# Kernel tuning notes

Measured on AMD Instinct MI355X. Metric: run time of the kernel, lower is better.

Reference implementation:

```python
import jax, jax.numpy as jnp
import numpy as np
from jax import lax

D_MODEL = 512
D_STATE = 64
D_CONV = 4
EXPAND = 2
HEADDIM = 64
D_INNER = EXPAND * D_MODEL          # 1024
NHEADS = D_INNER // HEADDIM         # 16
CONV_DIM = D_INNER + 2 * D_STATE    # 1152 (x, B, C go through depthwise conv)
D_PROJ = 2 * D_INNER + 2 * D_STATE + NHEADS  # 2192
EPS = 1e-5


def silu(x):
    return x * jax.nn.sigmoid(x)


def layernorm(x, w, b):
    mu = jnp.mean(x, axis=-1, keepdims=True)
    var = jnp.mean((x - mu) ** 2, axis=-1, keepdims=True)
    return (x - mu) * lax.rsqrt(var + EPS) * w + b


def mamba2(x, in_w, conv_w, conv_b, dt_bias, A_log, D_h, mnorm_w, out_w):
    """Faithful Mamba2 forward (sequential selective-scan form of SSD).
    x: [B, L, D_MODEL]"""
    Bsz, L, _ = x.shape
    zxbcdt = x @ in_w  # [B, L, D_PROJ]
    z = zxbcdt[..., :D_INNER]
    xBC = zxbcdt[..., D_INNER:D_INNER + CONV_DIM]
    dt = zxbcdt[..., -NHEADS:]

    # causal depthwise conv1d over sequence, then SiLU
    xBC_pad = jnp.pad(xBC, ((0, 0), (D_CONV - 1, 0), (0, 0)))
    xBC = lax.conv_general_dilated(
        xBC_pad, conv_w, window_strides=(1,), padding='VALID',
        dimension_numbers=('NWC', 'WIO', 'NWC'), feature_group_count=CONV_DIM)
    xBC = silu(xBC + conv_b)

    xh = xBC[..., :D_INNER].reshape(Bsz, L, NHEADS, HEADDIM)      # [B,L,H,P]
    Bc = xBC[..., D_INNER:D_INNER + D_STATE]                      # [B,L,N]
    Cc = xBC[..., D_INNER + D_STATE:]                             # [B,L,N]

    dt = jax.nn.softplus(dt + dt_bias)          # [B,L,H]
    dA = jnp.exp(dt * (-jnp.exp(A_log)))        # [B,L,H]
    dtx = dt[..., None] * xh                    # [B,L,H,P]

    def step(h, ins):
        dA_t, dtx_t, B_t, C_t = ins  # [B,H], [B,H,P], [B,N], [B,N]
        h = h * dA_t[:, :, None, None] + dtx_t[..., None] * B_t[:, None, None, :]
        y = jnp.einsum('bhpn,bn->bhp', h, C_t)
        return h, y

    h0 = jnp.zeros((Bsz, NHEADS, HEADDIM, D_STATE), x.dtype)
    xs = (jnp.moveaxis(dA, 1, 0), jnp.moveaxis(dtx, 1, 0),
          jnp.moveaxis(Bc, 1, 0), jnp.moveaxis(Cc, 1, 0))
    _, ys = lax.scan(step, h0, xs)              # [L,B,H,P]
    y = jnp.moveaxis(ys, 0, 1) + D_h[None, None, :, None] * xh
    y = y.reshape(Bsz, L, D_INNER)

    # gated RMSNorm: rmsnorm(y * silu(z)) * weight
    g = y * silu(z)
    g = g * lax.rsqrt(jnp.mean(g * g, axis=-1, keepdims=True) + EPS) * mnorm_w
    return g @ out_w  # [B, L, D_MODEL]


def setup_inputs() -> dict:
    key = jax.random.key(0)
    ks = jax.random.split(key, 16)
    B, L = 2, 4096
    s = 0.02
    inp = {
        'x': jax.random.normal(ks[0], (B, L, D_MODEL), jnp.float32),
        'norm_in_w': jnp.ones((D_MODEL,), jnp.float32),
        'norm_in_b': jnp.zeros((D_MODEL,), jnp.float32),
        'norm_out_w': jnp.ones((D_MODEL,), jnp.float32),
        'norm_out_b': jnp.zeros((D_MODEL,), jnp.float32),
        'in_w': jax.random.normal(ks[1], (D_MODEL, D_PROJ), jnp.float32) * s,
        'conv_w': jax.random.normal(ks[2], (D_CONV, 1, CONV_DIM), jnp.float32) * 0.1,
        'conv_b': jnp.zeros((CONV_DIM,), jnp.float32),
        'dt_bias': jnp.log(jnp.expm1(jax.random.uniform(ks[3], (NHEADS,), jnp.float32, 0.001, 0.1))),
        'A_log': jnp.log(jnp.arange(1, NHEADS + 1, dtype=jnp.float32)),
        'D_h': jnp.ones((NHEADS,), jnp.float32),
        'mnorm_w': jnp.ones((D_INNER,), jnp.float32),
        'out_w': jax.random.normal(ks[4], (D_INNER, D_MODEL), jnp.float32) * s,
        'ff_w1': jax.random.normal(ks[5], (D_MODEL, 4 * D_MODEL), jnp.float32) * s,
        'ff_b1': jnp.zeros((4 * D_MODEL,), jnp.float32),
        'ff_w2': jax.random.normal(ks[6], (4 * D_MODEL, D_MODEL), jnp.float32) * s,
        'ff_b2': jnp.zeros((D_MODEL,), jnp.float32),
    }
    return inp


def reference(x, norm_in_w, norm_in_b, norm_out_w, norm_out_b, in_w, conv_w,
              conv_b, dt_bias, A_log, D_h, mnorm_w, out_w, ff_w1, ff_b1,
              ff_w2, ff_b2):
    xn = layernorm(x, norm_in_w, norm_in_b)
    fwd = mamba2(xn, in_w, conv_w, conv_b, dt_bias, A_log, D_h, mnorm_w, out_w)
    bwd = mamba2(jnp.flip(xn, axis=1), in_w, conv_w, conv_b, dt_bias, A_log,
                 D_h, mnorm_w, out_w)
    m = layernorm(fwd + jnp.flip(bwd, axis=1), norm_out_w, norm_out_b)
    ff = jax.nn.gelu(m @ ff_w1 + ff_b1, approximate=False) @ ff_w2 + ff_b2
    return ff + x
```

## Files before the change

kernel.cpp:

```cpp
#include <hip/hip_runtime.h>
#include <hip/hip_bf16.h>

#define LSEQ 4096
#define BSZ 2
#define DMODEL 512
#define DINNER 1024
#define DSTATE 64
#define NHEADS 16
#define CONVDIM 1152
#define DPROJ 2192
#define NPAD 2304
#define NTOK (BSZ*LSEQ)
#define NCH 64

typedef __attribute__((ext_vector_type(8))) short short8;
typedef __attribute__((ext_vector_type(4))) float f32x4;

__device__ inline unsigned short f2b(float v){
  unsigned int u = __builtin_bit_cast(unsigned int, v);
  unsigned int r = (u + 0x7FFFu + ((u >> 16) & 1u)) >> 16;
  return (unsigned short)r;
}
__device__ inline float b2f(unsigned short u){
  unsigned int x = ((unsigned int)u) << 16;
  return __builtin_bit_cast(float, x);
}
__device__ inline uint4 pack8(const float* v){
  uint4 pk;
  pk.x = (unsigned)f2b(v[0]) | ((unsigned)f2b(v[1])<<16);
  pk.y = (unsigned)f2b(v[2]) | ((unsigned)f2b(v[3])<<16);
  pk.z = (unsigned)f2b(v[4]) | ((unsigned)f2b(v[5])<<16);
  pk.w = (unsigned)f2b(v[6]) | ((unsigned)f2b(v[7])<<16);
  return pk;
}

#define GLL16(gp, lp) __builtin_amdgcn_global_load_lds( \
    (const __attribute__((address_space(1))) unsigned int*)(gp), \
    (__attribute__((address_space(3))) unsigned int*)(lp), 16, 0, 0)

__global__ __launch_bounds__(256) void wconv_t(const float* __restrict__ src,
    unsigned short* __restrict__ dst, int K, int Nsrc, int Npad){
  __shared__ float t[32][33];
  int n0 = blockIdx.x*32, k0 = blockIdx.y*32;
  int tx = threadIdx.x & 31, ty = threadIdx.x >> 5;
  for (int i=0;i<4;i++){
    int k = k0 + ty + i*8; int n = n0 + tx;
    t[ty + i*8][tx] = (n < Nsrc) ? src[(size_t)k*Nsrc + n] : 0.f;
  }
  __syncthreads();
  for (int i=0;i<4;i++){
    int n = n0 + ty + i*8; int k = k0 + tx;
    if (n < Npad) dst[(size_t)n*K + k] = f2b(t[tx][ty + i*8]);
  }
}

__global__ __launch_bounds__(256) void layernorm_k(const float* __restrict__ in,
    const float* __restrict__ w, const float* __restrict__ bb, unsigned short* __restrict__ out){
  int row = blockIdx.x; int tid = threadIdx.x;
  const float* r = in + (size_t)row*DMODEL;
  float v0 = r[tid], v1 = r[tid+256];
  float s = v0+v1, sq = v0*v0+v1*v1;
  for (int m=32;m>=1;m>>=1){ s += __shfl_xor(s,m); sq += __shfl_xor(sq,m); }
  __shared__ float ws_[4], wq_[4];
  int wave = tid>>6, lane = tid&63;
  if (lane==0){ ws_[wave]=s; wq_[wave]=sq; }
  __syncthreads();
  s = ws_[0]+ws_[1]+ws_[2]+ws_[3]; sq = wq_[0]+wq_[1]+wq_[2]+wq_[3];
  float mu = s * (1.f/DMODEL);
  float var = sq * (1.f/DMODEL) - mu*mu;
  float rs = rsqrtf(var + 1e-5f);
  out[(size_t)row*DMODEL + tid]     = f2b((v0-mu)*rs*w[tid] + bb[tid]);
  out[(size_t)row*DMODEL + tid+256] = f2b((v1-mu)*rs*w[tid+256] + bb[tid+256]);
}

__global__ __launch_bounds__(256) void gemm_k(const unsigned short* __restrict__ A,
    const unsigned short* __restrict__ Bt, void* __restrict__ outp,
    int M, int N, int K, int epi, const float* __restrict__ bias, const float* __restrict__ resid){
  __shared__ __align__(16) unsigned short smem[8320];
  unsigned short* As = smem;
  unsigned short* Bs = smem + 128*32;
  int tid = threadIdx.x;
  int lane = tid & 63, wave = tid >> 6;
  int wr = wave >> 1, wc = wave & 1;
  int l15 = lane & 15, q = lane >> 4;
  int bm = blockIdx.y, bn = blockIdx.x;
  f32x4 acc[4][4];
  for (int i=0;i<4;i++) for(int j=0;j<4;j++) acc[i][j] = (f32x4){0.f,0.f,0.f,0.f};
  const size_t abase = (size_t)bm*128*K;
  const size_t bbase = (size_t)bn*128*K;
  for (int k0 = 0; k0 < K; k0 += 32){
    #pragma unroll
    for (int i=0;i<2;i++){
      int idx = tid + i*256; int rr = idx>>2, cg = idx&3;
      GLL16(A  + abase + (size_t)rr*K + k0 + cg*8, As + idx*8);
      GLL16(Bt + bbase + (size_t)rr*K + k0 + cg*8, Bs + idx*8);
    }
    __syncthreads();
    short8 af[4], bfr[4];
    for (int mt=0;mt<4;mt++) af[mt]  = *(const short8*)(&As[(wr*64+mt*16+l15)*32 + q*8]);
    for (int nt=0;nt<4;nt++) bfr[nt] = *(const short8*)(&Bs[(wc*64+nt*16+l15)*32 + q*8]);
    for (int mt=0;mt<4;mt++)
      for (int nt=0;nt<4;nt++)
        acc[mt][nt] = __builtin_amdgcn_mfma_f32_16x16x32_bf16(af[mt], bfr[nt], acc[mt][nt], 0,0,0);
    __syncthreads();
  }
  float* cbuf = ((float*)smem) + wave*1040;
  int rbase = q*4;
  int gr0t = bm*128 + wr*64;
  int gc0 = bn*128 + wc*64;
  for (int mt=0; mt<4; mt++){
    for (int nt=0;nt<4;nt++)
      for (int rr=0;rr<4;rr++)
        cbuf[(rbase+rr)*65 + nt*16 + l15] = acc[mt][nt][rr];
    int gr0 = gr0t + mt*16;
    if (epi == 1 || epi == 3){
      int r8 = lane >> 3, c0 = (lane & 7)*8;
      #pragma unroll
      for (int h=0; h<2; h++){
        int row = h*8 + r8;
        float v[8];
        #pragma unroll
        for (int t=0;t<8;t++) v[t] = cbuf[row*65 + c0 + t];
        if (epi == 1){
          #pragma unroll
          for (int t=0;t<8;t++){
            float bv = v[t] + bias[gc0 + c0 + t];
            v[t] = 0.5f*bv*(1.f+erff(bv*0.70710678118654752f));
          }
        }
        *(uint4*)((unsigned short*)outp + (size_t)(gr0+row)*N + gc0 + c0) = pack8(v);
      }
    } else {
      int r4 = lane >> 4, c0 = (lane & 15)*4;
      #pragma unroll
      for (int h=0; h<4; h++){
        int row = h*4 + r4;
        float4 v;
        v.x = cbuf[row*65 + c0 + 0];
        v.y = cbuf[row*65 + c0 + 1];
        v.z = cbuf[row*65 + c0 + 2];
        v.w = cbuf[row*65 + c0 + 3];
        if (epi == 2){
          const float4 rv = *(const float4*)(resid + (size_t)(gr0+row)*N + gc0 + c0);
          v.x += bias[gc0+c0+0] + rv.x;
          v.y += bias[gc0+c0+1] + rv.y;
          v.z += bias[gc0+c0+2] + rv.z;
          v.w += bias[gc0+c0+3] + rv.w;
        }
        *(float4*)((float*)outp + (size_t)(gr0+row)*N + gc0 + c0) = v;
      }
    }
  }
}

__global__ __launch_bounds__(256) void dt_k(const unsigned short* __restrict__ zx,
    const float* __restrict__ dt_bias, const float* __restrict__ A_log,
    float* __restrict__ dAb, float* __restrict__ dtb){
  int b = blockIdx.y;
  int t = blockIdx.x*16 + (threadIdx.x>>4);
  int h = threadIdx.x & 15;
  float raw = b2f(zx[((size_t)b*LSEQ + t)*NPAD + (DINNER+CONVDIM) + h]) + dt_bias[h];
  float dt = (raw > 20.f) ? raw : log1pf(expf(raw));
  float dA = expf(-expf(A_log[h]) * dt);
  size_t f = ((size_t)b*LSEQ + t)*NHEADS + h;
  size_t r = ((size_t)(BSZ+b)*LSEQ + (LSEQ-1-t))*NHEADS + h;
  dAb[f] = dA; dtb[f] = dt;
  dAb[r] = dA; dtb[r] = dt;
}

__global__ __launch_bounds__(256) void conv_x_k(const unsigned short* __restrict__ zx,
    const float* __restrict__ conv_w, const float* __restrict__ conv_b,
    const float* __restrict__ dtb, unsigned short* __restrict__ dtxb,
    unsigned short* __restrict__ zcomp){
  int b = blockIdx.y;
  int t0blk = blockIdx.x * 32;
  int tid = threadIdx.x;
  int half = tid >> 7, cg = tid & 127;
  int c0 = cg * 8;
  int head = c0 >> 6;
  float wk[4][8], bias8[8];
  #pragma unroll
  for (int k=0;k<4;k++)
    #pragma unroll
    for (int j=0;j<8;j++) wk[k][j] = conv_w[k*CONVDIM + c0 + j];
  #pragma unroll
  for (int j=0;j<8;j++) bias8[j] = conv_b[c0 + j];
  __shared__ float sdtf[32][16], sdtb[32][16];
  for (int r = tid; r < 512; r += 256){
    int i = r >> 4, h = r & 15;
    sdtf[i][h] = dtb[((size_t)b*LSEQ + t0blk + i)*NHEADS + h];
    sdtb[i][h] = dtb[((size_t)(BSZ+b)*LSEQ + (LSEQ-1-(t0blk+i)))*NHEADS + h];
  }
  __syncthreads();
  int t0 = t0blk + half*16;
  float w0[8],w1[8],w2[8],w3[8];
  #pragma unroll
  for (int j=0;j<8;j++){ w1[j]=0.f; w2[j]=0.f; w3[j]=0.f; }
  for (int it=0; it<22; ++it){
    int t = t0 - 3 + it;
    #pragma unroll
    for (int j=0;j<8;j++){ w0[j]=w1[j]; w1[j]=w2[j]; w2[j]=w3[j]; }
    if (t >= 0 && t < LSEQ){
      uint4 xv = *(const uint4*)(zx + ((size_t)b*LSEQ + t)*NPAD + DINNER + c0);
      const unsigned short* xs = (const unsigned short*)&xv;
      #pragma unroll
      for (int j=0;j<8;j++) w3[j] = b2f(xs[j]);
      if (t >= t0 && t < t0+16){
        uint4 zv = *(const uint4*)(zx + ((size_t)b*LSEQ + t)*NPAD + c0);
        *(uint4*)(zcomp + ((size_t)b*LSEQ + t)*DINNER + c0) = zv;
      }
    } else {
      #pragma unroll
      for (int j=0;j<8;j++) w3[j] = 0.f;
    }
    if (t >= t0 && t < t0+16){
      float dtf = sdtf[t - t0blk][head];
      float v[8];
      #pragma unroll
      for (int j=0;j<8;j++){
        float a = bias8[j] + wk[0][j]*w0[j] + wk[1][j]*w1[j] + wk[2][j]*w2[j] + wk[3][j]*w3[j];
        v[j] = (a / (1.f + expf(-a))) * dtf;
      }
      *(uint4*)(dtxb + ((size_t)b*LSEQ + t)*DINNER + c0) = pack8(v);
    }
    int tau = t - 3;
    if (tau >= t0 && tau < t0+16){
      float dtv = sdtb[tau - t0blk][head];
      float v[8];
      #pragma unroll
      for (int j=0;j<8;j++){
        float a = bias8[j] + wk[0][j]*w3[j] + wk[1][j]*w2[j] + wk[2][j]*w1[j] + wk[3][j]*w0[j];
        v[j] = (a / (1.f + expf(-a))) * dtv;
      }
      *(uint4*)(dtxb + ((size_t)(BSZ+b)*LSEQ + (LSEQ-1-tau))*DINNER + c0) = pack8(v);
    }
  }
}

__global__ __launch_bounds__(256) void conv_bc_k(const unsigned short* __restrict__ zx,
    const float* __restrict__ conv_w, const float* __restrict__ conv_b,
    unsigned short* __restrict__ Bb, unsigned short* __restrict__ Cb){
  int b = blockIdx.y;
  int t0blk = blockIdx.x * 64;
  int tid = threadIdx.x;
  int slot = tid >> 4, cg = tid & 15;
  int c0 = cg*8;
  int ccol = DINNER + 1024 + c0;
  int cw = 1024 + c0;
  float wk[4][8], bias8[8];
  #pragma unroll
  for (int k=0;k<4;k++)
    #pragma unroll
    for (int j=0;j<8;j++) wk[k][j] = conv_w[k*CONVDIM + cw + j];
  #pragma unroll
  for (int j=0;j<8;j++) bias8[j] = conv_b[cw + j];
  int t0 = t0blk + slot*4;
  float w0[8],w1[8],w2[8],w3[8];
  #pragma unroll
  for (int j=0;j<8;j++){ w1[j]=0.f; w2[j]=0.f; w3[j]=0.f; }
  for (int it=0; it<10; ++it){
    int t = t0 - 3 + it;
    #pragma unroll
    for (int j=0;j<8;j++){ w0[j]=w1[j]; w1[j]=w2[j]; w2[j]=w3[j]; }
    if (t >= 0 && t < LSEQ){
      uint4 xv = *(const uint4*)(zx + ((size_t)b*LSEQ + t)*NPAD + ccol);
      const unsigned short* xs = (const unsigned short*)&xv;
      #pragma unroll
      for (int j=0;j<8;j++) w3[j] = b2f(xs[j]);
    } else {
      #pragma unroll
      for (int j=0;j<8;j++) w3[j] = 0.f;
    }
    if (t >= t0 && t < t0+4){
      float v[8];
      #pragma unroll
      for (int j=0;j<8;j++){
        float a = bias8[j] + wk[0][j]*w0[j] + wk[1][j]*w1[j] + wk[2][j]*w2[j] + wk[3][j]*w3[j];
        v[j] = a / (1.f + expf(-a));
      }
      size_t tok = (size_t)b*LSEQ + t;
      if (c0 < 64) *(uint4*)(Bb + tok*DSTATE + c0)      = pack8(v);
      else         *(uint4*)(Cb + tok*DSTATE + (c0-64)) = pack8(v);
    }
    int tau = t - 3;
    if (tau >= t0 && tau < t0+4){
      float v[8];
      #pragma unroll
      for (int j=0;j<8;j++){
        float a = bias8[j] + wk[0][j]*w3[j] + wk[1][j]*w2[j] + wk[2][j]*w1[j] + wk[3][j]*w0[j];
        v[j] = a / (1.f + expf(-a));
      }
      size_t tok = (size_t)(BSZ+b)*LSEQ + (LSEQ-1-tau);
      if (c0 < 64) *(uint4*)(Bb + tok*DSTATE + c0)      = pack8(v);
      else         *(uint4*)(Cb + tok*DSTATE + (c0-64)) = pack8(v);
    }
  }
}

__device__ inline void gemm64(const unsigned short* Ab, const unsigned short* Bb_,
                              int l15, int q, f32x4 acc[4][4]){
  #pragma unroll
  for (int ks=0; ks<2; ks++){
    short8 af[4], bf4[4];
    #pragma unroll
    for (int mt=0;mt<4;mt++) af[mt]  = *(const short8*)(Ab  + (mt*16+l15)*72 + ks*32 + q*8);
    #pragma unroll
    for (int nt=0;nt<4;nt++) bf4[nt] = *(const short8*)(Bb_ + (nt*16+l15)*72 + ks*32 + q*8);
    #pragma unroll
    for (int mt=0;mt<4;mt++)
      #pragma unroll
      for (int nt=0;nt<4;nt++)
        acc[mt][nt] = __builtin_amdgcn_mfma_f32_16x16x32_bf16(af[mt], bf4[nt], acc[mt][nt], 0,0,0);
  }
}

__global__ __launch_bounds__(64) void ssd1_k(const float* __restrict__ dAb,
    const unsigned short* __restrict__ dtxb, const unsigned short* __restrict__ Bb,
    const unsigned short* __restrict__ Cb,
    unsigned short* __restrict__ y0, unsigned short* __restrict__ y1,
    unsigned short* __restrict__ hbuf, float* __restrict__ Pch, float* __restrict__ ebuf){
  int ch = blockIdx.x, h = blockIdx.y, z = blockIdx.z;
  int d = z >> 1, b = z & 1;
  int lane = threadIdx.x;
  int l15 = lane & 15, q = lane >> 4;
  int tr = lane >> 3, cb8 = (lane & 7)*8;
  size_t tokb = (size_t)z*LSEQ + (size_t)ch*64;
  size_t zhc = ((size_t)z*NHEADS + h)*NCH + ch;
  __shared__ __align__(16) unsigned short S1[64*72];
  __shared__ __align__(16) unsigned short S2[64*72];
  __shared__ __align__(16) unsigned short S3[64*72];
  __shared__ float Lb[64];
  float L = fmaxf(logf(dAb[(tokb + lane)*NHEADS + h]), -60.f);
  #pragma unroll
  for (int off=1; off<64; off<<=1){
    float v = __shfl_up(L, off);
    if (lane >= off) L += v;
  }
  Lb[lane] = L;
  float e = expf(L);
  ebuf[zhc*64 + lane] = e;
  if (lane == 63) Pch[zhc] = e;
  for (int i=0;i<8;i++){
    int t = i*8 + tr;
    *(uint4*)&S1[t*72 + cb8] = *(const uint4*)(Cb + (tokb+t)*DSTATE + cb8);
    *(uint4*)&S2[t*72 + cb8] = *(const uint4*)(Bb + (tokb+t)*DSTATE + cb8);
    uint4 xv = *(const uint4*)(dtxb + (tokb+t)*DINNER + (size_t)h*64 + cb8);
    const unsigned short* xs = (const unsigned short*)&xv;
    #pragma unroll
    for (int j=0;j<8;j++) S3[(cb8+j)*72 + t] = xs[j];
  }
  f32x4 sa[4][4];
  for (int i=0;i<4;i++) for (int j=0;j<4;j++) sa[i][j] = (f32x4){0.f,0.f,0.f,0.f};
  gemm64(S1, S2, l15, q, sa);
  float Lsv[4];
  #pragma unroll
  for (int nt=0;nt<4;nt++) Lsv[nt] = Lb[nt*16 + l15];
  #pragma unroll
  for (int mt=0;mt<4;mt++){
    #pragma unroll
    for (int r=0;r<4;r++){
      int t = mt*16 + q*4 + r;
      float Lt = Lb[t];
      #pragma unroll
      for (int nt=0;nt<4;nt++){
        int s = nt*16 + l15;
        float v = (t >= s) ? expf(Lt - Lsv[nt]) * sa[mt][nt][r] : 0.f;
        S1[t*72 + s] = f2b(v);
      }
    }
  }
  f32x4 ya[4][4];
  for (int i=0;i<4;i++) for (int j=0;j<4;j++) ya[i][j] = (f32x4){0.f,0.f,0.f,0.f};
  gemm64(S1, S3, l15, q, ya);
  #pragma unroll
  for (int mt=0;mt<4;mt++)
    #pragma unroll
    for (int pt=0;pt<4;pt++)
      #pragma unroll
      for (int r=0;r<4;r++)
        S2[(mt*16+q*4+r)*72 + pt*16 + l15] = f2b(ya[mt][pt][r]);
  unsigned short* yb = d ? y1 : y0;
  for (int i=0;i<8;i++){
    int t = i*8 + tr; int g = ch*64 + t;
    int tph = d ? (LSEQ-1-g) : g;
    *(uint4*)(yb + ((size_t)b*LSEQ + tph)*DINNER + (size_t)h*64 + cb8) = *(uint4*)&S2[t*72 + cb8];
  }
  float L63 = Lb[63];
  for (int i=0;i<8;i++){
    int s = i*8 + tr;
    float w = expf(L63 - Lb[s]);
    uint4 bv = *(const uint4*)(Bb + (tokb+s)*DSTATE + cb8);
    const unsigned short* bs = (const unsigned short*)&bv;
    #pragma unroll
    for (int j=0;j<8;j++) S2[(cb8+j)*72 + s] = f2b(w * b2f(bs[j]));
  }
  f32x4 ga[4][4];
  for (int i=0;i<4;i++) for (int j=0;j<4;j++) ga[i][j] = (f32x4){0.f,0.f,0.f,0.f};
  gemm64(S3, S2, l15, q, ga);
  #pragma unroll
  for (int pt=0;pt<4;pt++)
    #pragma unroll
    for (int nt=0;nt<4;nt++)
      #pragma unroll
      for (int r=0;r<4;r++)
        S1[(pt*16+q*4+r)*72 + nt*16 + l15] = f2b(ga[pt][nt][r]);
  for (int i=0;i<8;i++){
    int p = i*8 + tr;
    *(uint4*)(hbuf + zhc*4096 + (size_t)p*64 + cb8) = *(uint4*)&S1[p*72 + cb8];
  }
}

__global__ __launch_bounds__(256) void comb_k(unsigned short* __restrict__ hbuf,
    const float* __restrict__ Pch){
  int u = blockIdx.x; int tid = threadIdx.x;
  float hreg[16];
  #pragma unroll
  for (int k=0;k<16;k++) hreg[k]=0.f;
  for (int ch=0; ch<NCH; ch++){
    size_t base = ((size_t)u*NCH + ch)*4096;
    float P = Pch[(size_t)u*NCH + ch];
    #pragma unroll
    for (int k=0;k<16;k++){
      float t = b2f(hbuf[base + tid + k*256]);
      hbuf[base + tid + k*256] = f2b(hreg[k]);
      hreg[k] = hreg[k]*P + t;
    }
  }
}

__global__ __launch_bounds__(64) void ssd2_k(const unsigned short* __restrict__ Cb,
    const unsigned short* __restrict__ hbuf, const unsigned short* __restrict__ dtxb,
    const float* __restrict__ dtb, const float* __restrict__ ebuf, const float* __restrict__ Dh,
    unsigned short* __restrict__ y0, unsigned short* __restrict__ y1){
  int ch = blockIdx.x, h = blockIdx.y, z = blockIdx.z;
  int d = z >> 1, b = z & 1;
  int lane = threadIdx.x;
  int l15 = lane & 15, q = lane >> 4;
  int tr = lane >> 3, cb8 = (lane & 7)*8;
  size_t tokb = (size_t)z*LSEQ + (size_t)ch*64;
  size_t zhc = ((size_t)z*NHEADS + h)*NCH + ch;
  __shared__ __align__(16) unsigned short S1[64*72];
  __shared__ __align__(16) unsigned short S2[64*72];
  __shared__ __align__(16) unsigned short S3[64*72];
  __shared__ float eb2[64], dti[64];
  eb2[lane] = ebuf[zhc*64 + lane];
  dti[lane] = 1.f / dtb[(tokb + lane)*NHEADS + h];
  float Dv = Dh[h];
  for (int i=0;i<8;i++){
    int t = i*8 + tr;
    *(uint4*)&S1[t*72 + cb8] = *(const uint4*)(Cb + (tokb+t)*DSTATE + cb8);
    *(uint4*)&S2[t*72 + cb8] = *(const uint4*)(hbuf + zhc*4096 + (size_t)t*64 + cb8);
  }
  f32x4 acc[4][4];
  for (int i=0;i<4;i++) for (int j=0;j<4;j++) acc[i][j] = (f32x4){0.f,0.f,0.f,0.f};
  gemm64(S1, S2, l15, q, acc);
  unsigned short* yb = d ? y1 : y0;
  #pragma unroll
  for (int mt=0;mt<4;mt++){
    #pragma unroll
    for (int r=0;r<4;r++){
      int t = mt*16 + q*4 + r; int g = ch*64 + t;
      int tph = d ? (LSEQ-1-g) : g;
      size_t rowb = ((size_t)b*LSEQ + tph)*DINNER + (size_t)h*64;
      size_t dxb_ = (tokb + t)*DINNER + (size_t)h*64;
      float et = eb2[t], di = dti[t];
      #pragma unroll
      for (int pt=0;pt<4;pt++){
        int p = pt*16 + l15;
        float v = acc[mt][pt][r]*et + b2f(yb[rowb + p]) + Dv * b2f(dtxb[dxb_ + p]) * di;
        S3[t*72 + p] = f2b(v);
      }
    }
  }
  for (int i=0;i<8;i++){
    int t = i*8 + tr; int g = ch*64 + t;
    int tph = d ? (LSEQ-1-g) : g;
    *(uint4*)(yb + ((size_t)b*LSEQ + tph)*DINNER + (size_t)h*64 + cb8) = *(uint4*)&S3[t*72 + cb8];
  }
}

__global__ __launch_bounds__(256) void gate_k(const unsigned short* __restrict__ y0,
    const unsigned short* __restrict__ y1, const unsigned short* __restrict__ zcomp,
    const float* __restrict__ mnw, unsigned short* __restrict__ gsum){
  int tok = blockIdx.x; int tid = threadIdx.x;
  __shared__ float g0s[DINNER], g1s[DINNER];
  float ss0 = 0.f, ss1 = 0.f;
  for (int i=0;i<4;i++){
    int c = tid + i*256;
    float z = b2f(zcomp[(size_t)tok*DINNER + c]);
    float sz = z / (1.f + expf(-z));
    float g0 = b2f(y0[(size_t)tok*DINNER + c]) * sz;
    float g1 = b2f(y1[(size_t)tok*DINNER + c]) * sz;
    g0s[c] = g0; g1s[c] = g1;
    ss0 += g0*g0; ss1 += g1*g1;
  }
  for (int m=32;m>=1;m>>=1){ ss0 += __shfl_xor(ss0,m); ss1 += __shfl_xor(ss1,m); }
  __shared__ float w0[4], w1[4];
  int wave = tid>>6, lane = tid&63;
  if (lane==0){ w0[wave]=ss0; w1[wave]=ss1; }
  __syncthreads();
  ss0 = w0[0]+w0[1]+w0[2]+w0[3];
  ss1 = w1[0]+w1[1]+w1[2]+w1[3];
  float r0 = rsqrtf(ss0*(1.f/DINNER) + 1e-5f);
  float r1 = rsqrtf(ss1*(1.f/DINNER) + 1e-5f);
  for (int i=0;i<4;i++){
    int c = tid + i*256;
    gsum[(size_t)tok*DINNER + c] = f2b((g0s[c]*r0 + g1s[c]*r1) * mnw[c]);
  }
}

extern "C" void kernel_launch(void* const* d_in, const int* in_sizes, int n_in,
                              void* d_out, int out_size, void* d_ws, size_t ws_size,
                              hipStream_t stream){
  const float* x       = (const float*)d_in[0];
  const float* nin_w   = (const float*)d_in[1];
  const float* nin_b   = (const float*)d_in[2];
  const float* nout_w  = (const float*)d_in[3];
  const float* nout_b  = (const float*)d_in[4];
  const float* in_w    = (const float*)d_in[5];
  const float* conv_w  = (const float*)d_in[6];
  const float* conv_b  = (const float*)d_in[7];
  const float* dt_bias = (const float*)d_in[8];
  const float* A_log   = (const float*)d_in[9];
  const float* D_h     = (const float*)d_in[10];
  const float* mnorm_w = (const float*)d_in[11];
  const float* out_w   = (const float*)d_in[12];
  const float* ff_w1   = (const float*)d_in[13];
  const float* ff_b1   = (const float*)d_in[14];
  const float* ff_w2   = (const float*)d_in[15];
  const float* ff_b2   = (const float*)d_in[16];
  float* out = (float*)d_out;

  char* ws = (char*)d_ws;
  size_t off = 0;
  auto alloc = [&](size_t bytes)->char*{
    char* p = ws + off; off = (off + bytes + 255) & ~(size_t)255; return p; };
  unsigned short* xn_bf = (unsigned short*)alloc((size_t)NTOK*DMODEL*2);
  unsigned short* in_wT = (unsigned short*)alloc((size_t)NPAD*DMODEL*2);
  unsigned short* out_wT= (unsigned short*)alloc((size_t)DMODEL*DINNER*2);
  unsigned short* w1T   = (unsigned short*)alloc((size_t)2048*DMODEL*2);
  unsigned short* w2T   = (unsigned short*)alloc((size_t)DMODEL*2048*2);
  unsigned short* zx    = (unsigned short*)alloc((size_t)NTOK*NPAD*2);
  unsigned short* zcomp = (unsigned short*)alloc((size_t)NTOK*DINNER*2);
  float*          dAb   = (float*)alloc((size_t)2*NTOK*NHEADS*4);
  float*          dtb   = (float*)alloc((size_t)2*NTOK*NHEADS*4);
  unsigned short* Bb    = (unsigned short*)alloc((size_t)2*NTOK*DSTATE*2);
  unsigned short* Cb    = (unsigned short*)alloc((size_t)2*NTOK*DSTATE*2);
  unsigned short* dtxb  = (unsigned short*)alloc((size_t)2*NTOK*DINNER*2);
  unsigned short* y0    = (unsigned short*)alloc((size_t)NTOK*DINNER*2);
  unsigned short* y1    = (unsigned short*)alloc((size_t)NTOK*DINNER*2);
  float*          Pch   = (float*)alloc((size_t)64*NCH*4);
  float*          ebuf  = (float*)alloc((size_t)64*NCH*64*4);
  size_t need = off;
  if (need > ws_size) return;

  unsigned short* hbuf  = zx;
  unsigned short* gsum  = dtxb;
  float* mpre = (float*)(dtxb + (size_t)NTOK*DINNER);
  unsigned short* m_bf  = y0;
  unsigned short* h1    = zx;

  wconv_t<<<dim3(NPAD/32,   DMODEL/32), 256, 0, stream>>>(in_w,  in_wT,  DMODEL, DPROJ,  NPAD);
  wconv_t<<<dim3(DMODEL/32, DINNER/32), 256, 0, stream>>>(out_w, out_wT, DINNER, DMODEL, DMODEL);
  wconv_t<<<dim3(2048/32,   DMODEL/32), 256, 0, stream>>>(ff_w1, w1T,    DMODEL, 2048,   2048);
  wconv_t<<<dim3(DMODEL/32, 2048/32),   256, 0, stream>>>(ff_w2, w2T,    2048,   DMODEL, DMODEL);
  layernorm_k<<<NTOK, 256, 0, stream>>>(x, nin_w, nin_b, xn_bf);
  gemm_k<<<dim3(NPAD/128, NTOK/128), 256, 0, stream>>>(xn_bf, in_wT, zx, NTOK, NPAD, DMODEL, 3, nullptr, nullptr);
  dt_k<<<dim3(LSEQ/16, BSZ), 256, 0, stream>>>(zx, dt_bias, A_log, dAb, dtb);
  conv_x_k<<<dim3(LSEQ/32, BSZ), 256, 0, stream>>>(zx, conv_w, conv_b, dtb, dtxb, zcomp);
  conv_bc_k<<<dim3(LSEQ/64, BSZ), 256, 0, stream>>>(zx, conv_w, conv_b, Bb, Cb);
  ssd1_k<<<dim3(NCH, NHEADS, 2*BSZ), 64, 0, stream>>>(dAb, dtxb, Bb, Cb, y0, y1, hbuf, Pch, ebuf);
  comb_k<<<64, 256, 0, stream>>>(hbuf, Pch);
  ssd2_k<<<dim3(NCH, NHEADS, 2*BSZ), 64, 0, stream>>>(Cb, hbuf, dtxb, dtb, ebuf, D_h, y0, y1);
  gate_k<<<NTOK, 256, 0, stream>>>(y0, y1, zcomp, mnorm_w, gsum);
  gemm_k<<<dim3(DMODEL/128, NTOK/128), 256, 0, stream>>>(gsum, out_wT, mpre, NTOK, DMODEL, DINNER, 0, nullptr, nullptr);
  layernorm_k<<<NTOK, 256, 0, stream>>>(mpre, nout_w, nout_b, m_bf);
  gemm_k<<<dim3(2048/128, NTOK/128), 256, 0, stream>>>(m_bf, w1T, h1, NTOK, 2048, DMODEL, 1, ff_b1, nullptr);
  gemm_k<<<dim3(DMODEL/128, NTOK/128), 256, 0, stream>>>(h1, w2T, out, NTOK, DMODEL, 2048, 2, ff_b2, x);
}
```

Measured before the change: 455.2 us.

## Add 256x256 pipelined GEMM, tanh GELU, and split comb_k across blocks

Adds a 512-thread GEMM with 256x256 tiles, double-buffered LDS fed by direct global-to-LDS loads, block swizzling and interleaved MFMA phases. It is used for the in-projection and FF1 GEMMs to raise data reuse. The exact erf GELU is swapped for a tanh approximation built on a fast exp, which makes the epilogue cheaper but changes numerics slightly. comb_k is split over four times as many blocks so the sequential chunk scan runs with more parallelism.

```diff
diff --git a/kernel.cpp b/kernel.cpp
--- a/kernel.cpp
+++ b/kernel.cpp
@@ -32,6 +32,15 @@
   pk.z = (unsigned)f2b(v[4]) | ((unsigned)f2b(v[5])<<16);
   pk.w = (unsigned)f2b(v[6]) | ((unsigned)f2b(v[7])<<16);
   return pk;
+}
+__device__ inline float gelu_f(float x){
+  float x2 = x*x;
+  float u = x*(0.7978845608f + 0.0356774081f*x2);
+  float au = fabsf(u);
+  float z = __expf(-2.f*au);
+  float t = (1.f - z)/(1.f + z);
+  t = (u >= 0.f) ? t : -t;
+  return 0.5f*x*(1.f + t);
 }
 
 #define GLL16(gp, lp) __builtin_amdgcn_global_load_lds( \
@@ -123,10 +132,7 @@
         for (int t=0;t<8;t++) v[t] = cbuf[row*65 + c0 + t];
         if (epi == 1){
           #pragma unroll
-          for (int t=0;t<8;t++){
-            float bv = v[t] + bias[gc0 + c0 + t];
-            v[t] = 0.5f*bv*(1.f+erff(bv*0.70710678118654752f));
-          }
+          for (int t=0;t<8;t++) v[t] = gelu_f(v[t] + bias[gc0 + c0 + t]);
         }
         *(uint4*)((unsigned short*)outp + (size_t)(gr0+row)*N + gc0 + c0) = pack8(v);
       }
@@ -149,6 +155,146 @@
         }
         *(float4*)((float*)outp + (size_t)(gr0+row)*N + gc0 + c0) = v;
       }
+    }
+  }
+}
+
+__global__ __launch_bounds__(512, 2) void gemm256_k(const unsigned short* __restrict__ A,
+    const unsigned short* __restrict__ Bt, unsigned short* __restrict__ outp,
+    int M, int N, int K, int epi, const float* __restrict__ bias){
+  __shared__ __align__(16) unsigned short As[32768];
+  __shared__ __align__(16) unsigned short Bs[32768];
+  const int tid = threadIdx.x;
+  const int lane = tid & 63, wave = tid >> 6;
+  const int wr = wave >> 2, wc = wave & 3;
+  const int l15 = lane & 15, q = lane >> 4;
+  int nbx = gridDim.x;
+  int bid = blockIdx.y * nbx + blockIdx.x;
+  int cpx = (nbx * gridDim.y) >> 3;
+  int swz = (bid & 7) * cpx + (bid >> 3);
+  int bn = swz % nbx, bm = swz / nbx;
+  const int NT = K >> 6;
+  const int j0 = tid, j1 = tid + 512;
+  const int rr0 = j0 >> 2, rr1 = j1 >> 2;
+  const int sc0 = (j0 & 3) ^ ((rr0 >> 1) & 3);
+  const int sc1 = (j1 & 3) ^ ((rr1 >> 1) & 3);
+  const unsigned short* a0 = A  + (size_t)(bm*256 + rr0)*K + sc0*8;
+  const unsigned short* a1 = A  + (size_t)(bm*256 + rr1)*K + sc1*8;
+  const unsigned short* b0 = Bt + (size_t)(bn*256 + rr0)*K + sc0*8;
+  const unsigned short* b1 = Bt + (size_t)(bn*256 + rr1)*K + sc1*8;
+  unsigned short* lA0 = As + j0*8;
+  unsigned short* lA1 = As + j1*8;
+  unsigned short* lB0 = Bs + j0*8;
+  unsigned short* lB1 = Bs + j1*8;
+#define STGA(t,kh) { const int go=(t)*64+(kh)*32, lo=((t)&1)*16384+(kh)*8192; \
+  GLL16(a0+go, lA0+lo); GLL16(a1+go, lA1+lo); }
+#define STGB(t,kh) { const int go=(t)*64+(kh)*32, lo=((t)&1)*16384+(kh)*8192; \
+  GLL16(b0+go, lB0+lo); GLL16(b1+go, lB1+lo); }
+  f32x4 acc[8][4];
+  #pragma unroll
+  for (int i=0;i<8;i++)
+    #pragma unroll
+    for (int j=0;j<4;j++) acc[i][j] = (f32x4){0.f,0.f,0.f,0.f};
+  STGA(0,0); STGB(0,0); STGA(0,1); STGB(0,1);
+  STGA(1,0); STGB(1,0);
+  asm volatile("s_waitcnt vmcnt(4)" ::: "memory");
+  __builtin_amdgcn_s_barrier();
+  const int cOfs = (q ^ ((l15 >> 1) & 3)) * 8;
+  const int arow = wr*128 + l15;
+  const int brow = wc*64  + l15;
+  for (int t = 0; t < NT; ++t){
+    const unsigned short* Ab = As + (t & 1)*16384;
+    const unsigned short* Bb = Bs + (t & 1)*16384;
+    short8 af[4], bf4[4];
+    #pragma unroll
+    for (int mi=0;mi<4;mi++) af[mi]  = *(const short8*)(Ab + (arow + mi*16)*32 + cOfs);
+    #pragma unroll
+    for (int nt=0;nt<4;nt++) bf4[nt] = *(const short8*)(Bb + (brow + nt*16)*32 + cOfs);
+    if (t+1 < NT) STGA(t+1,1);
+    __builtin_amdgcn_s_barrier();
+    asm volatile("s_waitcnt lgkmcnt(0)" ::: "memory");
+    __builtin_amdgcn_sched_barrier(0);
+    __builtin_amdgcn_s_setprio(1);
+    #pragma unroll
+    for (int mi=0;mi<4;mi++)
+      #pragma unroll
+      for (int nt=0;nt<4;nt++)
+        acc[mi][nt] = __builtin_amdgcn_mfma_f32_16x16x32_bf16(af[mi], bf4[nt], acc[mi][nt], 0,0,0);
+    __builtin_amdgcn_s_setprio(0);
+    __builtin_amdgcn_s_barrier();
+    #pragma unroll
+    for (int mi=0;mi<4;mi++) af[mi] = *(const short8*)(Ab + (arow + (4+mi)*16)*32 + cOfs);
+    if (t+1 < NT) STGB(t+1,1);
+    __builtin_amdgcn_s_barrier();
+    asm volatile("s_waitcnt lgkmcnt(0)" ::: "memory");
+    __builtin_amdgcn_sched_barrier(0);
+    __builtin_amdgcn_s_setprio(1);
+    #pragma unroll
+    for (int mi=0;mi<4;mi++)
+      #pragma unroll
+      for (int nt=0;nt<4;nt++)
+        acc[4+mi][nt] = __builtin_amdgcn_mfma_f32_16x16x32_bf16(af[mi], bf4[nt], acc[4+mi][nt], 0,0,0);
+    __builtin_amdgcn_s_setprio(0);
+    __builtin_amdgcn_s_barrier();
+    #pragma unroll
+    for (int mi=0;mi<4;mi++) af[mi]  = *(const short8*)(Ab + 8192 + (arow + mi*16)*32 + cOfs);
+    #pragma unroll
+    for (int nt=0;nt<4;nt++) bf4[nt] = *(const short8*)(Bb + 8192 + (brow + nt*16)*32 + cOfs);
+    if (t+2 < NT) STGA(t+2,0);
+    __builtin_amdgcn_s_barrier();
+    asm volatile("s_waitcnt lgkmcnt(0)" ::: "memory");
+    __builtin_amdgcn_sched_barrier(0);
+    __builtin_amdgcn_s_setprio(1);
+    #pragma unroll
+    for (int mi=0;mi<4;mi++)
+      #pragma unroll
+      for (int nt=0;nt<4;nt++)
+        acc[mi][nt] = __builtin_amdgcn_mfma_f32_16x16x32_bf16(af[mi], bf4[nt], acc[mi][nt], 0,0,0);
+    __builtin_amdgcn_s_setprio(0);
+    __builtin_amdgcn_s_barrier();
+    #pragma unroll
+    for (int mi=0;mi<4;mi++) af[mi] = *(const short8*)(Ab + 8192 + (arow + (4+mi)*16)*32 + cOfs);
+    if (t+2 < NT) STGB(t+2,0);
+    __builtin_amdgcn_s_barrier();
+    asm volatile("s_waitcnt lgkmcnt(0)" ::: "memory");
+    __builtin_amdgcn_sched_barrier(0);
+    __builtin_amdgcn_s_setprio(1);
+    #pragma unroll
+    for (int mi=0;mi<4;mi++)
+      #pragma unroll
+      for (int nt=0;nt<4;nt++)
+        acc[4+mi][nt] = __builtin_amdgcn_mfma_f32_16x16x32_bf16(af[mi], bf4[nt], acc[4+mi][nt], 0,0,0);
+    __builtin_amdgcn_s_setprio(0);
+    if (t+2 < NT)      { asm volatile("s_waitcnt vmcnt(4)" ::: "memory"); }
+    else if (t+1 < NT) { asm volatile("s_waitcnt vmcnt(0)" ::: "memory"); }
+    __builtin_amdgcn_s_barrier();
+  }
+#undef STGA
+#undef STGB
+  float* cb = (float*)As + wave*1040;
+  const int rbase = q*4;
+  const int gr0t = bm*256 + wr*128;
+  const int gc0 = bn*256 + wc*64;
+  const int r8 = lane >> 3, c0 = (lane & 7)*8;
+  #pragma unroll
+  for (int mt=0; mt<8; mt++){
+    #pragma unroll
+    for (int nt=0;nt<4;nt++)
+      #pragma unroll
+      for (int r=0;r<4;r++)
+        cb[(rbase+r)*65 + nt*16 + l15] = acc[mt][nt][r];
+    int gr0 = gr0t + mt*16;
+    #pragma unroll
+    for (int h=0; h<2; h++){
+      int row = h*8 + r8;
+      float v[8];
+      #pragma unroll
+      for (int u=0;u<8;u++) v[u] = cb[row*65 + c0 + u];
+      if (epi == 1){
+        #pragma unroll
+        for (int u=0;u<8;u++) v[u] = gelu_f(v[u] + bias[gc0 + c0 + u]);
+      }
+      *(uint4*)(outp + (size_t)(gr0+row)*N + gc0 + c0) = pack8(v);
     }
   }
 }
@@ -413,16 +559,18 @@
 __global__ __launch_bounds__(256) void comb_k(unsigned short* __restrict__ hbuf,
     const float* __restrict__ Pch){
   int u = blockIdx.x; int tid = threadIdx.x;
-  float hreg[16];
-  #pragma unroll
-  for (int k=0;k<16;k++) hreg[k]=0.f;
+  int kb = blockIdx.y * 4;
+  float hreg[4];
+  #pragma unroll
+  for (int k=0;k<4;k++) hreg[k]=0.f;
   for (int ch=0; ch<NCH; ch++){
     size_t base = ((size_t)u*NCH + ch)*4096;
     float P = Pch[(size_t)u*NCH + ch];
     #pragma unroll
-    for (int k=0;k<16;k++){
-      float t = b2f(hbuf[base + tid + k*256]);
-      hbuf[base + tid + k*256] = f2b(hreg[k]);
+    for (int k=0;k<4;k++){
+      size_t idx = base + tid + (size_t)(kb+k)*256;
+      float t = b2f(hbuf[idx]);
+      hbuf[idx] = f2b(hreg[k]);
       hreg[k] = hreg[k]*P + t;
     }
   }
@@ -565,16 +713,16 @@
   wconv_t<<<dim3(2048/32,   DMODEL/32), 256, 0, stream>>>(ff_w1, w1T,    DMODEL, 2048,   2048);
   wconv_t<<<dim3(DMODEL/32, 2048/32),   256, 0, stream>>>(ff_w2, w2T,    2048,   DMODEL, DMODEL);
   layernorm_k<<<NTOK, 256, 0, stream>>>(x, nin_w, nin_b, xn_bf);
-  gemm_k<<<dim3(NPAD/128, NTOK/128), 256, 0, stream>>>(xn_bf, in_wT, zx, NTOK, NPAD, DMODEL, 3, nullptr, nullptr);
+  gemm256_k<<<dim3(NPAD/256, NTOK/256), 512, 0, stream>>>(xn_bf, in_wT, zx, NTOK, NPAD, DMODEL, 3, nullptr);
   dt_k<<<dim3(LSEQ/16, BSZ), 256, 0, stream>>>(zx, dt_bias, A_log, dAb, dtb);
   conv_x_k<<<dim3(LSEQ/32, BSZ), 256, 0, stream>>>(zx, conv_w, conv_b, dtb, dtxb, zcomp);
   conv_bc_k<<<dim3(LSEQ/64, BSZ), 256, 0, stream>>>(zx, conv_w, conv_b, Bb, Cb);
   ssd1_k<<<dim3(NCH, NHEADS, 2*BSZ), 64, 0, stream>>>(dAb, dtxb, Bb, Cb, y0, y1, hbuf, Pch, ebuf);
-  comb_k<<<64, 256, 0, stream>>>(hbuf, Pch);
+  comb_k<<<dim3(64, 4), 256, 0, stream>>>(hbuf, Pch);
   ssd2_k<<<dim3(NCH, NHEADS, 2*BSZ), 64, 0, stream>>>(Cb, hbuf, dtxb, dtb, ebuf, D_h, y0, y1);
   gate_k<<<NTOK, 256, 0, stream>>>(y0, y1, zcomp, mnorm_w, gsum);
   gemm_k<<<dim3(DMODEL/128, NTOK/128), 256, 0, stream>>>(gsum, out_wT, mpre, NTOK, DMODEL, DINNER, 0, nullptr, nullptr);
   layernorm_k<<<NTOK, 256, 0, stream>>>(mpre, nout_w, nout_b, m_bf);
-  gemm_k<<<dim3(2048/128, NTOK/128), 256, 0, stream>>>(m_bf, w1T, h1, NTOK, 2048, DMODEL, 1, ff_b1, nullptr);
+  gemm256_k<<<dim3(2048/256, NTOK/256), 512, 0, stream>>>(m_bf, w1T, h1, NTOK, 2048, DMODEL, 1, ff_b1);
   gemm_k<<<dim3(DMODEL/128, NTOK/128), 256, 0, stream>>>(h1, w2T, out, NTOK, DMODEL, 2048, 2, ff_b2, x);
 }
```

Measured after the change: 429.6 us. -5.6%, faster.
